# Kernel tuning notes

Hardware: AMD Instinct MI355X
Metric: run time of the kernel (lower is better)

The kernel has to match this reference:

```python
import jax, jax.numpy as jnp
import numpy as np

N, D, E = 32768, 768, 8
F = 4 * D  # 3072


def setup_inputs() -> dict:
    key = jax.random.key(0)
    ks = jax.random.split(key, 8)
    scale = 0.02
    hidden_states = jax.random.normal(ks[0], (N, D), dtype=jnp.float32)
    Wg = jax.random.normal(ks[1], (E, D), dtype=jnp.float32) * scale  # gate, no bias
    W1 = jax.random.normal(ks[2], (E, F, D), dtype=jnp.float32) * scale
    b1 = jnp.zeros((E, F), dtype=jnp.float32)
    W2 = jax.random.normal(ks[3], (E, D, F), dtype=jnp.float32) * scale
    b2 = jnp.zeros((E, D), dtype=jnp.float32)
    W3 = jax.random.normal(ks[4], (E, 1, D), dtype=jnp.float32) * scale
    b3 = jnp.zeros((E, 1), dtype=jnp.float32)
    return {"hidden_states": hidden_states, "Wg": Wg, "W1": W1, "b1": b1,
            "W2": W2, "b2": b2, "W3": W3, "b3": b3, "top_k": 2}


def reference(hidden_states, Wg, W1, b1, W2, b2, W3, b3, top_k):
    x = hidden_states  # [N, D]
    logits = x @ Wg.T  # [N, E]
    probs = jax.nn.softmax(logits.astype(jnp.float32), axis=-1)
    w, _sel = jax.lax.top_k(probs, top_k)  # [N, k] (descending)
    w = (w / w.sum(axis=-1, keepdims=True)).astype(x.dtype)
    # FAITHFUL TO SOURCE BUG: expert used is the position index j (experts[j]),
    # not the selected expert id. So densely run experts 0..top_k-1 on all tokens.
    W1k, b1k = W1[:top_k], b1[:top_k]
    W2k, b2k = W2[:top_k], b2[:top_k]
    W3k, b3k = W3[:top_k], b3[:top_k]
    # dropout is identity in eval mode
    h = jax.nn.relu(jnp.einsum('nd,kfd->knf', x, W1k) + b1k[:, None, :])  # [k,N,F]
    o = x[None, :, :] + jnp.einsum('knf,kdf->knd', h, W2k) + b2k[:, None, :]  # residual, [k,N,D]
    s = jnp.einsum('knd,kod->kno', o, W3k) + b3k[:, None, :]  # [k,N,1]
    out = jnp.sum(jnp.swapaxes(w, 0, 1)[:, :, None] * s, axis=0)  # [N,1]
    return out
```

## Files before the change

kernel.cpp:

```cpp
#include <hip/hip_runtime.h>
#include <hip/hip_bf16.h>
#include <stdint.h>

#define N_TOK 32768
#define DDIM  768
#define FDIM  3072
#define NCOLS (2*FDIM)
#define BK    64
#define KTILES (DDIM/BK)
#define NTILES (NCOLS/256)
#define VD_CHUNK 96

typedef __attribute__((ext_vector_type(8))) short bf16x8;
typedef __attribute__((ext_vector_type(4))) float f32x4;

__device__ __forceinline__ unsigned short f2bf(float f) {
  unsigned u = __builtin_bit_cast(unsigned, f);
  unsigned r = (u + 0x7fffu + ((u >> 16) & 1u)) >> 16;
  return (unsigned short)r;
}

__device__ __forceinline__ void gl_lds16(const void* g, void* l) {
  __builtin_amdgcn_global_load_lds(
      (const __attribute__((address_space(1))) unsigned int*)g,
      (__attribute__((address_space(3))) unsigned int*)l, 16, 0, 0);
}

__global__ __launch_bounds__(256) void cvt_kernel(const float* __restrict__ src,
                                                  unsigned short* __restrict__ dst) {
  size_t i = ((size_t)blockIdx.x * 256 + threadIdx.x) * 4;
  float4 f = *(const float4*)(src + i);
  ushort4 u;
  u.x = f2bf(f.x); u.y = f2bf(f.y); u.z = f2bf(f.z); u.w = f2bf(f.w);
  *(ushort4*)(dst + i) = u;
}

__global__ __launch_bounds__(256) void vcalc_kernel(const float* __restrict__ W2,
                                                    const float* __restrict__ W3,
                                                    float* __restrict__ vpart) {
  __shared__ float w3s[VD_CHUNK];
  int k  = blockIdx.x / 12;
  int fb = blockIdx.x % 12;
  int db = blockIdx.y;
  if (threadIdx.x < VD_CHUNK) w3s[threadIdx.x] = W3[k*DDIM + db*VD_CHUNK + threadIdx.x];
  __syncthreads();
  int f = fb*256 + threadIdx.x;
  const float* W2k = W2 + (size_t)k*DDIM*FDIM + (size_t)db*VD_CHUNK*FDIM + f;
  float s = 0.f;
  #pragma unroll 8
  for (int d = 0; d < VD_CHUNK; ++d) s += W2k[(size_t)d*FDIM] * w3s[d];
  vpart[(size_t)db*NCOLS + k*FDIM + f] = s;
}

__global__ __launch_bounds__(256) void vfinal_kernel(const float* __restrict__ vpart,
                                                     float* __restrict__ v,
                                                     const float* __restrict__ b2,
                                                     const float* __restrict__ W3,
                                                     const float* __restrict__ b3,
                                                     float* __restrict__ cbuf) {
  int f = blockIdx.x*256 + threadIdx.x;
  float s = 0.f;
  #pragma unroll
  for (int db = 0; db < 8; ++db) s += vpart[(size_t)db*NCOLS + f];
  v[f] = s;
  if (blockIdx.x == 0 && threadIdx.x < 128) {
    int k = threadIdx.x >> 6, lane = threadIdx.x & 63;
    float c = 0.f;
    #pragma unroll
    for (int it = 0; it < DDIM/64; ++it) {
      int i = it*64 + lane;
      c += b2[k*DDIM + i] * W3[k*DDIM + i];
    }
    #pragma unroll
    for (int m = 1; m < 64; m <<= 1) c += __shfl_xor(c, m, 64);
    if (lane == 0) cbuf[k] = c + b3[k];
  }
}

__global__ __launch_bounds__(256) void gate_cvt_kernel(
    const float* __restrict__ x, const float* __restrict__ Wg,
    const float* __restrict__ W3, const float* __restrict__ cbuf,
    unsigned short* __restrict__ xbf,
    float* __restrict__ wgt, float* __restrict__ base) {
  int wid  = threadIdx.x >> 6;
  int lane = threadIdx.x & 63;
  int n = blockIdx.x * 4 + wid;
  const float4* xr = (const float4*)(x + (size_t)n * DDIM);
  ushort4* xw = (ushort4*)(xbf + (size_t)n * DDIM);
  float acc[8] = {0,0,0,0,0,0,0,0};
  float d30 = 0.f, d31 = 0.f;
  #pragma unroll
  for (int it = 0; it < DDIM/256; ++it) {
    int i = it*64 + lane;
    float4 xv = xr[i];
    ushort4 u;
    u.x = f2bf(xv.x); u.y = f2bf(xv.y); u.z = f2bf(xv.z); u.w = f2bf(xv.w);
    xw[i] = u;
    #pragma unroll
    for (int e = 0; e < 8; ++e) {
      float4 w = ((const float4*)(Wg + e*DDIM))[i];
      acc[e] += xv.x*w.x + xv.y*w.y + xv.z*w.z + xv.w*w.w;
    }
    float4 wa = ((const float4*)W3)[i];
    d30 += xv.x*wa.x + xv.y*wa.y + xv.z*wa.z + xv.w*wa.w;
    float4 wb = ((const float4*)(W3 + DDIM))[i];
    d31 += xv.x*wb.x + xv.y*wb.y + xv.z*wb.z + xv.w*wb.w;
  }
  #pragma unroll
  for (int m = 1; m < 64; m <<= 1) {
    #pragma unroll
    for (int e = 0; e < 8; ++e) acc[e] += __shfl_xor(acc[e], m, 64);
    d30 += __shfl_xor(d30, m, 64);
    d31 += __shfl_xor(d31, m, 64);
  }
  if (lane == 0) {
    float l1 = acc[0]; int a1 = 0;
    #pragma unroll
    for (int e = 1; e < 8; ++e) if (acc[e] > l1) { l1 = acc[e]; a1 = e; }
    float l2 = -3.4e38f;
    #pragma unroll
    for (int e = 0; e < 8; ++e) if (e != a1 && acc[e] > l2) l2 = acc[e];
    float w0 = 1.f / (1.f + __expf(l2 - l1));
    float w1 = 1.f - w0;
    wgt[2*n]   = w0;
    wgt[2*n+1] = w1;
    base[n] = w0 * (d30 + cbuf[0]) + w1 * (d31 + cbuf[1]);
  }
}

__global__ __launch_bounds__(512, 2) void gemm_kernel(
    const unsigned short* __restrict__ A,
    const unsigned short* __restrict__ B,
    const float* __restrict__ b1,
    const float* __restrict__ v,
    float* __restrict__ part) {
  __shared__ __align__(16) char smem[131072];

  const int tid  = threadIdx.x;
  const int lane = tid & 63, wid = tid >> 6;
  const int wm = wid >> 2, wn = wid & 3;
  const int q  = lane >> 4, cl = lane & 15;
  const int bn = blockIdx.x;
  const int bm = blockIdx.y;

  const unsigned short* Ab = A + (size_t)bm * 256 * DDIM;
  const unsigned short* Bb = B + (size_t)bn * 256 * DDIM;

  const size_t srow = (size_t)(wid*16 + cl) * DDIM + q*8;

  const int lb = lane * 16;
  const int aBase = wm*8192 + lb;
  const int bBase = 16384 + wn*4096 + lb;

  f32x4 zero = {0.f, 0.f, 0.f, 0.f};
  f32x4 acc[8][4];
  #pragma unroll
  for (int i = 0; i < 8; ++i)
    #pragma unroll
    for (int j = 0; j < 4; ++j) acc[i][j] = zero;

  auto stageA = [&](int t, int ks) {
    char* dst = smem + (t & 1) * 65536 + ks * 32768;
    const unsigned short* s0 = Ab + srow + t*BK + ks*32;
    gl_lds16(s0,            dst + wid*1024);
    gl_lds16(s0 + 128*DDIM, dst + 8192 + wid*1024);
  };
  auto stageB = [&](int t, int ks) {
    char* dst = smem + (t & 1) * 65536 + ks * 32768 + 16384;
    const unsigned short* s0 = Bb + srow + t*BK + ks*32;
    gl_lds16(s0,            dst + wid*1024);
    gl_lds16(s0 + 128*DDIM, dst + 8192 + wid*1024);
  };

  stageA(0, 0); stageB(0, 0);
  stageA(0, 1); stageB(0, 1);
  stageA(1, 0); stageB(1, 0);
  asm volatile("s_waitcnt vmcnt(8)" ::: "memory");
  __builtin_amdgcn_s_barrier();
  __builtin_amdgcn_sched_barrier(0);

  int buf = 0;
  #pragma unroll
  for (int kt = 0; kt < KTILES; ++kt) {
    const char* ct = smem + buf * 65536;
    bf16x8 af[4], bfr[4];

    #pragma unroll
    for (int n = 0; n < 4; ++n) bfr[n] = *(const bf16x8*)(ct + bBase + n*1024);
    #pragma unroll
    for (int m = 0; m < 4; ++m) af[m] = *(const bf16x8*)(ct + aBase + m*1024);
    if (kt <= 10) stageA(kt + 1, 1);
    __builtin_amdgcn_s_barrier();
    asm volatile("s_waitcnt lgkmcnt(0)" ::: "memory");
    __builtin_amdgcn_s_setprio(1);
    #pragma unroll
    for (int m = 0; m < 4; ++m)
      #pragma unroll
      for (int n = 0; n < 4; ++n)
        acc[m][n] = __builtin_amdgcn_mfma_f32_16x16x32_bf16(af[m], bfr[n], acc[m][n], 0, 0, 0);
    __builtin_amdgcn_s_setprio(0);
    __builtin_amdgcn_s_barrier();

    #pragma unroll
    for (int m = 0; m < 4; ++m) af[m] = *(const bf16x8*)(ct + aBase + 4096 + m*1024);
    if (kt <= 10) stageB(kt + 1, 1);
    __builtin_amdgcn_s_barrier();
    asm volatile("s_waitcnt lgkmcnt(0)" ::: "memory");
    __builtin_amdgcn_s_setprio(1);
    #pragma unroll
    for (int m = 0; m < 4; ++m)
      #pragma unroll
      for (int n = 0; n < 4; ++n)
        acc[4 + m][n] = __builtin_amdgcn_mfma_f32_16x16x32_bf16(af[m], bfr[n], acc[4 + m][n], 0, 0, 0);
    __builtin_amdgcn_s_setprio(0);
    if (kt <= 10) { asm volatile("s_waitcnt vmcnt(8)" ::: "memory"); }
    else          { asm volatile("s_waitcnt vmcnt(0)" ::: "memory"); }
    __builtin_amdgcn_s_barrier();
    __builtin_amdgcn_sched_barrier(0);

    #pragma unroll
    for (int n = 0; n < 4; ++n) bfr[n] = *(const bf16x8*)(ct + 32768 + bBase + n*1024);
    #pragma unroll
    for (int m = 0; m < 4; ++m) af[m] = *(const bf16x8*)(ct + 32768 + aBase + m*1024);
    if (kt <= 9) stageA(kt + 2, 0);
    __builtin_amdgcn_s_barrier();
    asm volatile("s_waitcnt lgkmcnt(0)" ::: "memory");
    __builtin_amdgcn_s_setprio(1);
    #pragma unroll
    for (int m = 0; m < 4; ++m)
      #pragma unroll
      for (int n = 0; n < 4; ++n)
        acc[m][n] = __builtin_amdgcn_mfma_f32_16x16x32_bf16(af[m], bfr[n], acc[m][n], 0, 0, 0);
    __builtin_amdgcn_s_setprio(0);
    __builtin_amdgcn_s_barrier();

    #pragma unroll
    for (int m = 0; m < 4; ++m) af[m] = *(const bf16x8*)(ct + 32768 + aBase + 4096 + m*1024);
    if (kt <= 9) stageB(kt + 2, 0);
    __builtin_amdgcn_s_barrier();
    asm volatile("s_waitcnt lgkmcnt(0)" ::: "memory");
    __builtin_amdgcn_s_setprio(1);
    #pragma unroll
    for (int m = 0; m < 4; ++m)
      #pragma unroll
      for (int n = 0; n < 4; ++n)
        acc[4 + m][n] = __builtin_amdgcn_mfma_f32_16x16x32_bf16(af[m], bfr[n], acc[4 + m][n], 0, 0, 0);
    __builtin_amdgcn_s_setprio(0);
    if (kt <= 9)        { asm volatile("s_waitcnt vmcnt(8)" ::: "memory"); }
    else if (kt == 10)  { asm volatile("s_waitcnt vmcnt(4)" ::: "memory"); }
    else                { asm volatile("s_waitcnt vmcnt(0)" ::: "memory"); }
    __builtin_amdgcn_s_barrier();
    __builtin_amdgcn_sched_barrier(0);

    buf ^= 1;
  }

  float vv[4], bb[4];
  #pragma unroll
  for (int n = 0; n < 4; ++n) {
    int cg = bn*256 + wn*64 + n*16 + cl;
    vv[n] = v[cg];
    bb[n] = b1[cg];
  }
  float* red = (float*)smem;
  #pragma unroll
  for (int mt = 0; mt < 8; ++mt) {
    #pragma unroll
    for (int rr = 0; rr < 4; ++rr) {
      float s = 0.f;
      #pragma unroll
      for (int n = 0; n < 4; ++n) {
        float val = acc[mt][n][rr] + bb[n];
        s += fmaxf(val, 0.f) * vv[n];
      }
      #pragma unroll
      for (int msk = 1; msk < 16; msk <<= 1) s += __shfl_xor(s, msk, 64);
      if (cl == 0) red[(wm*128 + mt*16 + q*4 + rr)*4 + wn] = s;
    }
  }
  __syncthreads();
  if (tid < 256) {
    float r4 = red[tid*4] + red[tid*4+1] + red[tid*4+2] + red[tid*4+3];
    part[(size_t)bn * N_TOK + (size_t)bm*256 + tid] = r4;
  }
}

__global__ __launch_bounds__(256) void final_kernel(const float* __restrict__ part,
                                                    const float* __restrict__ wgt,
                                                    const float* __restrict__ base,
                                                    float* __restrict__ out) {
  int n = blockIdx.x * 256 + threadIdx.x;
  float s0 = 0.f, s1 = 0.f;
  #pragma unroll
  for (int t = 0; t < 12; ++t) s0 += part[(size_t)t*N_TOK + n];
  #pragma unroll
  for (int t = 12; t < 24; ++t) s1 += part[(size_t)t*N_TOK + n];
  out[n] = base[n] + wgt[2*n]*s0 + wgt[2*n+1]*s1;
}

extern "C" void kernel_launch(void* const* d_in, const int* in_sizes, int n_in,
                              void* d_out, int out_size, void* d_ws, size_t ws_size,
                              hipStream_t stream) {
  const float* x  = (const float*)d_in[0];
  const float* Wg = (const float*)d_in[1];
  const float* W1 = (const float*)d_in[2];
  const float* b1 = (const float*)d_in[3];
  const float* W2 = (const float*)d_in[4];
  const float* b2 = (const float*)d_in[5];
  const float* W3 = (const float*)d_in[6];
  const float* b3 = (const float*)d_in[7];
  float* out = (float*)d_out;

  char* ws = (char*)d_ws;
  size_t off = 0;
  auto alloc = [&](size_t bytes) -> char* {
    char* p = ws + off;
    off += (bytes + 255) & ~(size_t)255;
    return p;
  };
  unsigned short* xbf  = (unsigned short*)alloc((size_t)N_TOK * DDIM * 2);
  unsigned short* w1bf = (unsigned short*)alloc((size_t)NCOLS * DDIM * 2);
  float* vpart = (float*)alloc((size_t)8 * NCOLS * 4);
  float* v     = (float*)alloc((size_t)NCOLS * 4);
  float* cbuf  = (float*)alloc(64);
  float* wgt   = (float*)alloc((size_t)N_TOK * 2 * 4);
  float* base  = (float*)alloc((size_t)N_TOK * 4);
  float* part  = (float*)alloc((size_t)NTILES * N_TOK * 4);
  if (off > ws_size) return;

  cvt_kernel<<<(NCOLS*DDIM)/1024, 256, 0, stream>>>(W1, w1bf);
  vcalc_kernel<<<dim3(24, 8), 256, 0, stream>>>(W2, W3, vpart);
  vfinal_kernel<<<NCOLS/256, 256, 0, stream>>>(vpart, v, b2, W3, b3, cbuf);
  gate_cvt_kernel<<<N_TOK/4, 256, 0, stream>>>(x, Wg, W3, cbuf, xbf, wgt, base);
  gemm_kernel<<<dim3(NTILES, N_TOK/256), 512, 0, stream>>>(xbf, w1bf, b1, v, part);
  final_kernel<<<N_TOK/256, 256, 0, stream>>>(part, wgt, base, out);
}
```

Baseline: 616.6 us.

## Remap GEMM blocks across XCDs and merge half-k MFMA phases with fewer barriers

The GEMM grid becomes a 1D launch of 3072 blocks, remapped so that consecutive logical tiles (sharing the same A row panel) land on the same XCD, with the aim of improving L2 reuse. The main loop also loads both A halves and B together, issues both staging copies at once, and runs all 32 MFMAs per k-slice between a single wait/barrier pair, halving the number of barriers and lgkm waits. This raises VGPR pressure (extra a1 fragment) and makes the LDS read-before-overwrite ordering depend on the remaining barrier placement.

```diff
diff --git a/kernel.cpp b/kernel.cpp
--- a/kernel.cpp
+++ b/kernel.cpp
@@ -140,8 +140,11 @@
   const int lane = tid & 63, wid = tid >> 6;
   const int wm = wid >> 2, wn = wid & 3;
   const int q  = lane >> 4, cl = lane & 15;
-  const int bn = blockIdx.x;
-  const int bm = blockIdx.y;
+
+  const int b  = blockIdx.x;
+  const int L  = (b & 7) * 384 + (b >> 3);
+  const int bn = L % 24;
+  const int bm = L / 24;
 
   const unsigned short* Ab = A + (size_t)bm * 256 * DDIM;
   const unsigned short* Bb = B + (size_t)bn * 256 * DDIM;
@@ -179,39 +182,29 @@
   __builtin_amdgcn_s_barrier();
   __builtin_amdgcn_sched_barrier(0);
 
-  int buf = 0;
   #pragma unroll
   for (int kt = 0; kt < KTILES; ++kt) {
-    const char* ct = smem + buf * 65536;
-    bf16x8 af[4], bfr[4];
-
-    #pragma unroll
-    for (int n = 0; n < 4; ++n) bfr[n] = *(const bf16x8*)(ct + bBase + n*1024);
-    #pragma unroll
-    for (int m = 0; m < 4; ++m) af[m] = *(const bf16x8*)(ct + aBase + m*1024);
-    if (kt <= 10) stageA(kt + 1, 1);
-    __builtin_amdgcn_s_barrier();
-    asm volatile("s_waitcnt lgkmcnt(0)" ::: "memory");
+    const char* ct = smem + (kt & 1) * 65536;
+    bf16x8 a0[4], a1[4], bf0[4];
+
+    #pragma unroll
+    for (int n = 0; n < 4; ++n) bf0[n] = *(const bf16x8*)(ct + bBase + n*1024);
+    #pragma unroll
+    for (int m = 0; m < 4; ++m) a0[m] = *(const bf16x8*)(ct + aBase + m*1024);
+    #pragma unroll
+    for (int m = 0; m < 4; ++m) a1[m] = *(const bf16x8*)(ct + aBase + 4096 + m*1024);
+    if (kt <= 10) { stageA(kt + 1, 1); stageB(kt + 1, 1); }
     __builtin_amdgcn_s_setprio(1);
     #pragma unroll
     for (int m = 0; m < 4; ++m)
       #pragma unroll
       for (int n = 0; n < 4; ++n)
-        acc[m][n] = __builtin_amdgcn_mfma_f32_16x16x32_bf16(af[m], bfr[n], acc[m][n], 0, 0, 0);
-    __builtin_amdgcn_s_setprio(0);
-    __builtin_amdgcn_s_barrier();
-
-    #pragma unroll
-    for (int m = 0; m < 4; ++m) af[m] = *(const bf16x8*)(ct + aBase + 4096 + m*1024);
-    if (kt <= 10) stageB(kt + 1, 1);
-    __builtin_amdgcn_s_barrier();
-    asm volatile("s_waitcnt lgkmcnt(0)" ::: "memory");
-    __builtin_amdgcn_s_setprio(1);
+        acc[m][n] = __builtin_amdgcn_mfma_f32_16x16x32_bf16(a0[m], bf0[n], acc[m][n], 0, 0, 0);
     #pragma unroll
     for (int m = 0; m < 4; ++m)
       #pragma unroll
       for (int n = 0; n < 4; ++n)
-        acc[4 + m][n] = __builtin_amdgcn_mfma_f32_16x16x32_bf16(af[m], bfr[n], acc[4 + m][n], 0, 0, 0);
+        acc[4 + m][n] = __builtin_amdgcn_mfma_f32_16x16x32_bf16(a1[m], bf0[n], acc[4 + m][n], 0, 0, 0);
     __builtin_amdgcn_s_setprio(0);
     if (kt <= 10) { asm volatile("s_waitcnt vmcnt(8)" ::: "memory"); }
     else          { asm volatile("s_waitcnt vmcnt(0)" ::: "memory"); }
@@ -219,40 +212,28 @@
     __builtin_amdgcn_sched_barrier(0);
 
     #pragma unroll
-    for (int n = 0; n < 4; ++n) bfr[n] = *(const bf16x8*)(ct + 32768 + bBase + n*1024);
-    #pragma unroll
-    for (int m = 0; m < 4; ++m) af[m] = *(const bf16x8*)(ct + 32768 + aBase + m*1024);
-    if (kt <= 9) stageA(kt + 2, 0);
-    __builtin_amdgcn_s_barrier();
-    asm volatile("s_waitcnt lgkmcnt(0)" ::: "memory");
+    for (int n = 0; n < 4; ++n) bf0[n] = *(const bf16x8*)(ct + 32768 + bBase + n*1024);
+    #pragma unroll
+    for (int m = 0; m < 4; ++m) a0[m] = *(const bf16x8*)(ct + 32768 + aBase + m*1024);
+    #pragma unroll
+    for (int m = 0; m < 4; ++m) a1[m] = *(const bf16x8*)(ct + 32768 + aBase + 4096 + m*1024);
+    if (kt <= 9) { stageA(kt + 2, 0); stageB(kt + 2, 0); }
     __builtin_amdgcn_s_setprio(1);
     #pragma unroll
     for (int m = 0; m < 4; ++m)
       #pragma unroll
       for (int n = 0; n < 4; ++n)
-        acc[m][n] = __builtin_amdgcn_mfma_f32_16x16x32_bf16(af[m], bfr[n], acc[m][n], 0, 0, 0);
+        acc[m][n] = __builtin_amdgcn_mfma_f32_16x16x32_bf16(a0[m], bf0[n], acc[m][n], 0, 0, 0);
+    #pragma unroll
+    for (int m = 0; m < 4; ++m)
+      #pragma unroll
+      for (int n = 0; n < 4; ++n)
+        acc[4 + m][n] = __builtin_amdgcn_mfma_f32_16x16x32_bf16(a1[m], bf0[n], acc[4 + m][n], 0, 0, 0);
     __builtin_amdgcn_s_setprio(0);
-    __builtin_amdgcn_s_barrier();
-
-    #pragma unroll
-    for (int m = 0; m < 4; ++m) af[m] = *(const bf16x8*)(ct + 32768 + aBase + 4096 + m*1024);
-    if (kt <= 9) stageB(kt + 2, 0);
-    __builtin_amdgcn_s_barrier();
-    asm volatile("s_waitcnt lgkmcnt(0)" ::: "memory");
-    __builtin_amdgcn_s_setprio(1);
-    #pragma unroll
-    for (int m = 0; m < 4; ++m)
-      #pragma unroll
-      for (int n = 0; n < 4; ++n)
-        acc[4 + m][n] = __builtin_amdgcn_mfma_f32_16x16x32_bf16(af[m], bfr[n], acc[4 + m][n], 0, 0, 0);
-    __builtin_amdgcn_s_setprio(0);
-    if (kt <= 9)        { asm volatile("s_waitcnt vmcnt(8)" ::: "memory"); }
-    else if (kt == 10)  { asm volatile("s_waitcnt vmcnt(4)" ::: "memory"); }
-    else                { asm volatile("s_waitcnt vmcnt(0)" ::: "memory"); }
+    if (kt <= 9)       { asm volatile("s_waitcnt vmcnt(8)" ::: "memory"); }
+    else if (kt == 10) { asm volatile("s_waitcnt vmcnt(4)" ::: "memory"); }
     __builtin_amdgcn_s_barrier();
     __builtin_amdgcn_sched_barrier(0);
-
-    buf ^= 1;
   }
 
   float vv[4], bb[4];
@@ -332,6 +313,6 @@
   vcalc_kernel<<<dim3(24, 8), 256, 0, stream>>>(W2, W3, vpart);
   vfinal_kernel<<<NCOLS/256, 256, 0, stream>>>(vpart, v, b2, W3, b3, cbuf);
   gate_cvt_kernel<<<N_TOK/4, 256, 0, stream>>>(x, Wg, W3, cbuf, xbf, wgt, base);
-  gemm_kernel<<<dim3(NTILES, N_TOK/256), 512, 0, stream>>>(xbf, w1bf, b1, v, part);
+  gemm_kernel<<<3072, 512, 0, stream>>>(xbf, w1bf, b1, v, part);
   final_kernel<<<N_TOK/256, 256, 0, stream>>>(part, wgt, base, out);
 }
```

Result: no change. 626.6 us (+1.6%).
